# Performance work log

Measured on AMD Instinct MI355X. Metric: run time of the kernel, lower is better.

The kernel has to match this reference:

```python
import jax, jax.numpy as jnp
import numpy as np

B, T, D = 4, 2048, 2048
NUM_HEADS = 16
NUM_KV_HEADS = 4
HEAD_DIM = D // NUM_HEADS  # 128
KV_GROUPS = NUM_HEADS // NUM_KV_HEADS  # 4
ROPE_THETA = 10000.0


def _rope_tables(seq_len, head_dim, theta):
    inv_freq = 1.0 / theta ** (jnp.arange(0, head_dim, 2, dtype=jnp.float32) / head_dim)
    t = jnp.arange(seq_len, dtype=jnp.float32)
    freqs = jnp.outer(t, inv_freq)  # (T, head_dim//2)
    return jnp.cos(freqs), jnp.sin(freqs)


def _apply_rotary(x, cos, sin):
    # x: (B, H, T, d); cos/sin: (T, d//2)
    d = x.shape[-1]
    x1, x2 = x[..., : d // 2], x[..., d // 2:]
    c = cos[None, None, :, :]
    s = sin[None, None, :, :]
    return jnp.concatenate([x1 * c - x2 * s, x1 * s + x2 * c], axis=-1)


def setup_inputs() -> dict:
    key = jax.random.key(0)
    kx, kq, kk, kv, ko = jax.random.split(key, 5)
    scale = 1.0 / np.sqrt(D)
    return {
        "x": jax.random.normal(kx, (B, T, D), dtype=jnp.float32),
        "Wq": jax.random.normal(kq, (NUM_HEADS * HEAD_DIM, D), dtype=jnp.float32) * scale,
        "Wk": jax.random.normal(kk, (NUM_KV_HEADS * HEAD_DIM, D), dtype=jnp.float32) * scale,
        "Wv": jax.random.normal(kv, (NUM_KV_HEADS * HEAD_DIM, D), dtype=jnp.float32) * scale,
        "Wo": jax.random.normal(ko, (D, D), dtype=jnp.float32) * scale,
    }


def reference(x, Wq, Wk, Wv, Wo):
    Bc, Tc, Dc = x.shape
    # projections (Linear with weight (out,in): y = x @ W.T)
    q = (x @ Wq.T).reshape(Bc, Tc, NUM_HEADS, HEAD_DIM).transpose(0, 2, 1, 3)
    k = (x @ Wk.T).reshape(Bc, Tc, NUM_KV_HEADS, HEAD_DIM).transpose(0, 2, 1, 3)
    v = (x @ Wv.T).reshape(Bc, Tc, NUM_KV_HEADS, HEAD_DIM).transpose(0, 2, 1, 3)

    cos, sin = _rope_tables(Tc, HEAD_DIM, ROPE_THETA)
    q = _apply_rotary(q, cos, sin)
    k = _apply_rotary(k, cos, sin)

    # grouped-query attention: broadcast KV heads instead of repeat_interleave
    # q: (B, kvH, G, T, d); k,v: (B, kvH, T, d)
    qg = q.reshape(Bc, NUM_KV_HEADS, KV_GROUPS, Tc, HEAD_DIM)
    scores = jnp.einsum("bkgtd,bksd->bkgts", qg, k) / jnp.sqrt(jnp.float32(HEAD_DIM))
    causal = jnp.tril(jnp.ones((Tc, Tc), dtype=bool))
    scores = jnp.where(causal[None, None, None], scores, jnp.float32(-jnp.inf))
    attn = jax.nn.softmax(scores, axis=-1)
    out = jnp.einsum("bkgts,bksd->bkgtd", attn, v)  # (B, kvH, G, T, d)
    out = out.reshape(Bc, NUM_HEADS, Tc, HEAD_DIM).transpose(0, 2, 1, 3).reshape(Bc, Tc, Dc)
    return out @ Wo.T
```

## Files before the change

kernel.cpp:

```cpp
#include <hip/hip_runtime.h>
#include <stdint.h>

#define B_ 4
#define T_ 2048
#define D_ 2048
#define NH_ 16
#define NKV_ 4
#define HD_ 128
#define QKVN 3072
#define QSCALE_ 0.1275174334161689f

typedef unsigned short u16;
typedef __attribute__((ext_vector_type(8))) short short8;
typedef __attribute__((ext_vector_type(4))) float floatx4;

typedef __attribute__((address_space(1))) void* gas_p;
typedef __attribute__((address_space(3))) void* las_p;

__device__ __forceinline__ u16 f2bf(float f) {
  union { float f; uint32_t u; } a; a.f = f;
  uint32_t r = a.u + 0x7fffu + ((a.u >> 16) & 1u);
  return (u16)(r >> 16);
}
__device__ __forceinline__ float bf2f(u16 u) {
  union { uint32_t u; float f; } a; a.u = ((uint32_t)u) << 16;
  return a.f;
}
__device__ __forceinline__ void gl_lds16(const u16* g, u16* l) {
  __builtin_amdgcn_global_load_lds((gas_p)g, (las_p)l, 16, 0, 0);
}

__global__ void cvt_kernel(const float* __restrict__ in, u16* __restrict__ out, int n) {
  int i = blockIdx.x * 256 + threadIdx.x;
  if (i * 4 >= n) return;
  float4 v = ((const float4*)in)[i];
  union { u16 u[4]; uint2 v2; } o;
  o.u[0] = f2bf(v.x); o.u[1] = f2bf(v.y); o.u[2] = f2bf(v.z); o.u[3] = f2bf(v.w);
  ((uint2*)out)[i] = o.v2;
}

__global__ void rope_tables_kernel(float* __restrict__ tabs) {
  int i = blockIdx.x * 256 + threadIdx.x;
  if (i >= T_ * 64) return;
  int t = i >> 6, d = i & 63;
  float inv = powf(10000.0f, -(float)d / 64.0f);
  float f = (float)t * inv;
  tabs[i] = cosf(f);
  tabs[T_ * 64 + i] = sinf(f);
}

__global__ void rope_q_kernel(const u16* __restrict__ qkv, const float* __restrict__ tabs,
                              u16* __restrict__ q_r) {
  int i = blockIdx.x * 256 + threadIdx.x;
  if (i >= B_ * T_ * NH_ * 64) return;
  int d = i & 63;
  int h = (i >> 6) & 15;
  int t = (i >> 10) & 2047;
  int b = i >> 21;
  size_t row = (size_t)(b * T_ + t) * QKVN + h * HD_;
  float x1 = bf2f(qkv[row + d]);
  float x2 = bf2f(qkv[row + d + 64]);
  float c = tabs[t * 64 + d];
  float s = tabs[T_ * 64 + t * 64 + d];
  size_t ob = ((size_t)(b * NH_ + h) * T_ + t) * HD_;
  q_r[ob + d] = f2bf((x1 * c - x2 * s) * QSCALE_);
  q_r[ob + d + 64] = f2bf((x1 * s + x2 * c) * QSCALE_);
}

__global__ void rope_k_kernel(const u16* __restrict__ qkv, const float* __restrict__ tabs,
                              u16* __restrict__ k_r) {
  int i = blockIdx.x * 256 + threadIdx.x;
  if (i >= B_ * T_ * NKV_ * 64) return;
  int d = i & 63;
  int kh = (i >> 6) & 3;
  int t = (i >> 8) & 2047;
  int b = i >> 19;
  size_t row = (size_t)(b * T_ + t) * QKVN + D_ + kh * HD_;
  float x1 = bf2f(qkv[row + d]);
  float x2 = bf2f(qkv[row + d + 64]);
  float c = tabs[t * 64 + d];
  float s = tabs[T_ * 64 + t * 64 + d];
  size_t ob = ((size_t)(b * NKV_ + kh) * T_ + t) * HD_;
  k_r[ob + d] = f2bf(x1 * c - x2 * s);
  k_r[ob + d + 64] = f2bf(x1 * s + x2 * c);
}

__global__ void v_trans_kernel(const u16* __restrict__ qkv, u16* __restrict__ v_t) {
  __shared__ u16 tile[64 * 128];
  int bk = blockIdx.y;
  int b = bk >> 2, kh = bk & 3;
  int t0 = blockIdx.x * 64;
#pragma unroll
  for (int rep = 0; rep < 32; rep++) {
    int idx = rep * 256 + threadIdx.x;
    int tt = idx >> 7, d = idx & 127;
    tile[idx] = qkv[(size_t)(b * T_ + t0 + tt) * QKVN + D_ + 512 + kh * HD_ + d];
  }
  __syncthreads();
#pragma unroll
  for (int rep = 0; rep < 32; rep++) {
    int idx = rep * 256 + threadIdx.x;
    int d = idx >> 6, tt = idx & 63;
    v_t[((size_t)bk * HD_ + d) * T_ + t0 + tt] = tile[tt * 128 + d];
  }
}

template <int OUTF32>
__global__ __launch_bounds__(256)
void gemm_bt(const u16* __restrict__ A, const u16* __restrict__ Bm,
             void* __restrict__ Cv, int M, int N, int K) {
  __shared__ u16 As[128 * 64];
  __shared__ u16 Bs[128 * 64];
  const int tid = threadIdx.x;
  const int wave = tid >> 6, lane = tid & 63;
  const int l16 = lane & 15, quad = lane >> 4;
  const int m0 = blockIdx.y * 128, n0 = blockIdx.x * 128;
  const int wm = (wave >> 1) * 64, wn = (wave & 1) * 64;

  floatx4 acc[4][4];
#pragma unroll
  for (int i = 0; i < 4; i++)
#pragma unroll
    for (int j = 0; j < 4; j++)
#pragma unroll
      for (int r = 0; r < 4; r++) acc[i][j][r] = 0.0f;

  const u16* gA[4]; const u16* gB[4]; u16* lA[4]; u16* lB[4];
#pragma unroll
  for (int rep = 0; rep < 4; rep++) {
    int u = rep * 256 + tid;
    int row = u >> 3;
    int ks = (u & 7) ^ (row & 7);
    gA[rep] = A + (size_t)(m0 + row) * K + ks * 8;
    gB[rep] = Bm + (size_t)(n0 + row) * K + ks * 8;
    lA[rep] = &As[u * 8];
    lB[rep] = &Bs[u * 8];
  }

  for (int k0 = 0; k0 < K; k0 += 64) {
#pragma unroll
    for (int rep = 0; rep < 4; rep++) {
      gl_lds16(gA[rep] + k0, lA[rep]);
      gl_lds16(gB[rep] + k0, lB[rep]);
    }
    __syncthreads();
#pragma unroll
    for (int kc = 0; kc < 2; kc++) {
      const int kq = (kc * 4 + quad) ^ (l16 & 7);
      short8 af[4], bfv[4];
#pragma unroll
      for (int i = 0; i < 4; i++)
        af[i] = *(const short8*)(As + ((wm + i * 16 + l16) * 8 + kq) * 8);
#pragma unroll
      for (int j = 0; j < 4; j++)
        bfv[j] = *(const short8*)(Bs + ((wn + j * 16 + l16) * 8 + kq) * 8);
#pragma unroll
      for (int i = 0; i < 4; i++)
#pragma unroll
        for (int j = 0; j < 4; j++)
          acc[i][j] = __builtin_amdgcn_mfma_f32_16x16x32_bf16(af[i], bfv[j], acc[i][j], 0, 0, 0);
    }
    __syncthreads();
  }
#pragma unroll
  for (int i = 0; i < 4; i++)
#pragma unroll
    for (int j = 0; j < 4; j++)
#pragma unroll
      for (int r = 0; r < 4; r++) {
        int m = m0 + wm + i * 16 + quad * 4 + r;
        int n = n0 + wn + j * 16 + l16;
        if (OUTF32)
          ((float*)Cv)[(size_t)m * N + n] = acc[i][j][r];
        else
          ((u16*)Cv)[(size_t)m * N + n] = f2bf(acc[i][j][r]);
      }
}

__global__ __launch_bounds__(256)
void attn_fused(const u16* __restrict__ q_r, const u16* __restrict__ k_r,
                const u16* __restrict__ v_t, u16* __restrict__ outp) {
  __shared__ u16 Ks[64 * 128];
  __shared__ u16 Vs[64 * 128];
  __shared__ u16 Ps[4][32 * 64];
  const int tid = threadIdx.x;
  const int wave = tid >> 6, lane = tid & 63;
  const int l16 = lane & 15, quad = lane >> 4;
  const int bh = blockIdx.y;
  const int b = bh >> 4, h = bh & 15;
  const int kh = h >> 2;

  const u16* qhead = q_r + (size_t)bh * T_ * HD_;
  const u16* khead = k_r + (size_t)(b * NKV_ + kh) * T_ * HD_;
  const u16* vhead = v_t + (size_t)(b * NKV_ + kh) * HD_ * T_;

  int uu[4], kv_j[4], kv_kb[4], v_jo[4], v_k2[4], nn16[4], qq[4];
#pragma unroll
  for (int rep = 0; rep < 4; rep++) {
    int u = rep * 256 + tid;
    uu[rep] = u;
    nn16[rep] = u & 15; qq[rep] = (u >> 4) & 3;
    kv_j[rep] = (u >> 6) & 3; kv_kb[rep] = (u >> 8) & 3;
    v_jo[rep] = (u >> 6) & 7; v_k2[rep] = (u >> 9) & 1;
  }

  const short8 ones = { 0x3F80, 0x3F80, 0x3F80, 0x3F80, 0x3F80, 0x3F80, 0x3F80, 0x3F80 };
  char* psb = (char*)&Ps[wave][0];
  const int swz = (l16 & 7) << 4;

  for (int pass = 0; pass < 2; pass++) {
    const int qtile = pass ? (15 - (int)blockIdx.x) : (int)blockIdx.x;
    const int qbase = qtile * 128;
    const int ntiles = 2 * qtile + 2;

    short8 qf[2][4];
#pragma unroll
    for (int i = 0; i < 2; i++) {
      int t = qbase + wave * 32 + i * 16 + l16;
#pragma unroll
      for (int kb = 0; kb < 4; kb++)
        qf[i][kb] = *(const short8*)(qhead + (size_t)t * HD_ + kb * 32 + quad * 8);
    }

    const u16* kg[4]; const u16* vg[4]; u16* kl[4]; u16* vl[4];
#pragma unroll
    for (int rep = 0; rep < 4; rep++) {
      kg[rep] = khead + (size_t)(kv_j[rep] * 16 + nn16[rep]) * HD_ + kv_kb[rep] * 32 + qq[rep] * 8;
      vg[rep] = vhead + (size_t)(v_jo[rep] * 16 + nn16[rep]) * T_ + v_k2[rep] * 32 + qq[rep] * 8;
      kl[rep] = &Ks[uu[rep] * 8];
      vl[rep] = &Vs[uu[rep] * 8];
    }

    floatx4 acc_o[2][8];
    floatx4 acc_l[2];
#pragma unroll
    for (int i = 0; i < 2; i++) {
#pragma unroll
      for (int jo = 0; jo < 8; jo++)
#pragma unroll
        for (int r = 0; r < 4; r++) acc_o[i][jo][r] = 0.0f;
#pragma unroll
      for (int r = 0; r < 4; r++) acc_l[i][r] = 0.0f;
    }

    for (int tile = 0; tile < ntiles; tile++) {
      const int kv0 = tile * 64;
#pragma unroll
      for (int rep = 0; rep < 4; rep++) {
        gl_lds16(kg[rep], kl[rep]);
        gl_lds16(vg[rep], vl[rep]);
        kg[rep] += 64 * HD_;
        vg[rep] += 64;
      }
      __syncthreads();

      floatx4 s_acc[2][4];
#pragma unroll
      for (int i = 0; i < 2; i++)
#pragma unroll
        for (int j = 0; j < 4; j++)
#pragma unroll
          for (int r = 0; r < 4; r++) s_acc[i][j][r] = 0.0f;
      __builtin_amdgcn_s_setprio(1);
#pragma unroll
      for (int kb = 0; kb < 4; kb++) {
        short8 bk[4];
#pragma unroll
        for (int j = 0; j < 4; j++)
          bk[j] = *(const short8*)(Ks + (((kb * 4 + j) * 4 + quad) * 16 + l16) * 8);
#pragma unroll
        for (int i = 0; i < 2; i++)
#pragma unroll
          for (int j = 0; j < 4; j++)
            s_acc[i][j] = __builtin_amdgcn_mfma_f32_16x16x32_bf16(bk[j], qf[i][kb], s_acc[i][j], 0, 0, 0);
      }
      __builtin_amdgcn_s_setprio(0);

      if (tile + 2 >= ntiles) {
#pragma unroll
        for (int i = 0; i < 2; i++) {
          const int qg = qbase + wave * 32 + i * 16 + l16;
          const int prow = i * 16 + l16;
#pragma unroll
          for (int j = 0; j < 4; j++) {
            const int kg0 = kv0 + j * 16 + quad * 4;
            float p0 = (kg0 + 0 > qg) ? 0.0f : exp2f(s_acc[i][j][0]);
            float p1 = (kg0 + 1 > qg) ? 0.0f : exp2f(s_acc[i][j][1]);
            float p2 = (kg0 + 2 > qg) ? 0.0f : exp2f(s_acc[i][j][2]);
            float p3 = (kg0 + 3 > qg) ? 0.0f : exp2f(s_acc[i][j][3]);
            uint32_t lo, hi;
            asm("v_cvt_pk_bf16_f32 %0, %1, %2" : "=v"(lo) : "v"(p0), "v"(p1));
            asm("v_cvt_pk_bf16_f32 %0, %1, %2" : "=v"(hi) : "v"(p2), "v"(p3));
            uint2 pk; pk.x = lo; pk.y = hi;
            *(uint2*)(psb + ((prow * 128 + j * 32 + quad * 8) ^ swz)) = pk;
          }
        }
      } else {
#pragma unroll
        for (int i = 0; i < 2; i++) {
          const int prow = i * 16 + l16;
#pragma unroll
          for (int j = 0; j < 4; j++) {
            float p0 = exp2f(s_acc[i][j][0]);
            float p1 = exp2f(s_acc[i][j][1]);
            float p2 = exp2f(s_acc[i][j][2]);
            float p3 = exp2f(s_acc[i][j][3]);
            uint32_t lo, hi;
            asm("v_cvt_pk_bf16_f32 %0, %1, %2" : "=v"(lo) : "v"(p0), "v"(p1));
            asm("v_cvt_pk_bf16_f32 %0, %1, %2" : "=v"(hi) : "v"(p2), "v"(p3));
            uint2 pk; pk.x = lo; pk.y = hi;
            *(uint2*)(psb + ((prow * 128 + j * 32 + quad * 8) ^ swz)) = pk;
          }
        }
      }

      __builtin_amdgcn_s_setprio(1);
#pragma unroll
      for (int k2 = 0; k2 < 2; k2++) {
        short8 ap[2];
#pragma unroll
        for (int i = 0; i < 2; i++) {
          const int prow = i * 16 + l16;
          ap[i] = *(const short8*)(psb + ((prow * 128 + k2 * 64 + quad * 16) ^ swz));
        }
#pragma unroll
        for (int jo = 0; jo < 8; jo++) {
          short8 bv = *(const short8*)(Vs + (((k2 * 8 + jo) * 4 + quad) * 16 + l16) * 8);
          acc_o[0][jo] = __builtin_amdgcn_mfma_f32_16x16x32_bf16(ap[0], bv, acc_o[0][jo], 0, 0, 0);
          acc_o[1][jo] = __builtin_amdgcn_mfma_f32_16x16x32_bf16(ap[1], bv, acc_o[1][jo], 0, 0, 0);
        }
        acc_l[0] = __builtin_amdgcn_mfma_f32_16x16x32_bf16(ap[0], ones, acc_l[0], 0, 0, 0);
        acc_l[1] = __builtin_amdgcn_mfma_f32_16x16x32_bf16(ap[1], ones, acc_l[1], 0, 0, 0);
      }
      __builtin_amdgcn_s_setprio(0);
      __syncthreads();
    }

#pragma unroll
    for (int i = 0; i < 2; i++)
#pragma unroll
      for (int r = 0; r < 4; r++) {
        const float inv = 1.0f / acc_l[i][r];
        const int t = qbase + wave * 32 + i * 16 + quad * 4 + r;
        u16* orow = outp + ((size_t)(b * T_ + t)) * D_ + h * HD_;
#pragma unroll
        for (int jo = 0; jo < 8; jo++)
          orow[jo * 16 + l16] = f2bf(acc_o[i][jo][r] * inv);
      }
    __syncthreads();
  }
}

extern "C" void kernel_launch(void* const* d_in, const int* in_sizes, int n_in,
                              void* d_out, int out_size, void* d_ws, size_t ws_size,
                              hipStream_t stream) {
  const float* x  = (const float*)d_in[0];
  const float* Wq = (const float*)d_in[1];
  const float* Wk = (const float*)d_in[2];
  const float* Wv = (const float*)d_in[3];
  const float* Wo = (const float*)d_in[4];

  char* ws = (char*)d_ws;
  u16* xbf  = (u16*)(ws);
  u16* attn = xbf;
  u16* qkv  = (u16*)(ws + 33554432);
  u16* wcat = (u16*)(ws + 83886080);
  u16* wobf = (u16*)(ws + 96468992);
  u16* qr   = (u16*)(ws + 104857600);
  u16* kr   = (u16*)(ws + 138412032);
  u16* vt   = (u16*)(ws + 146800640);
  float* tabs = (float*)(ws + 155189248);

  cvt_kernel<<<16384, 256, 0, stream>>>(x, xbf, 16777216);
  cvt_kernel<<<4096, 256, 0, stream>>>(Wq, wcat, 4194304);
  cvt_kernel<<<1024, 256, 0, stream>>>(Wk, wcat + 4194304, 1048576);
  cvt_kernel<<<1024, 256, 0, stream>>>(Wv, wcat + 5242880, 1048576);
  cvt_kernel<<<4096, 256, 0, stream>>>(Wo, wobf, 4194304);
  rope_tables_kernel<<<512, 256, 0, stream>>>(tabs);

  gemm_bt<0><<<dim3(24, 64), 256, 0, stream>>>(xbf, wcat, (void*)qkv, 8192, 3072, 2048);

  rope_q_kernel<<<32768, 256, 0, stream>>>(qkv, tabs, qr);
  rope_k_kernel<<<8192, 256, 0, stream>>>(qkv, tabs, kr);
  v_trans_kernel<<<dim3(32, 16), 256, 0, stream>>>(qkv, vt);

  attn_fused<<<dim3(8, 64), 256, 0, stream>>>(qr, kr, vt, attn);

  gemm_bt<1><<<dim3(16, 64), 256, 0, stream>>>(attn, wobf, d_out, 8192, 2048, 2048);
}
```

Before: 500.8 us.

## Use 256x256 double-buffered GEMM tiles with XCD-aware block swizzle

Replaces the 128x128 single-buffered projection GEMM with a 256x256 tile run by 512 threads (8 waves, each computing 128x64). The kernel double-buffers LDS so the next K-slice loads while the current one is multiplied, and drops one barrier per iteration. It also remaps block IDs so neighbouring tiles land on the same XCD, and raises wave priority around the MFMA burst. The goal is more reuse per loaded byte, better L2 locality and hidden load latency. In exchange, LDS use reaches 128 KB per block and register pressure rises, which limits occupancy, and the QKV GEMM grid shrinks to 384 blocks.

Measured after the change: 460.8 us. 1.09x faster.

```diff
diff --git a/kernel.cpp b/kernel.cpp
--- a/kernel.cpp
+++ b/kernel.cpp
@@ -106,64 +106,88 @@
 }
 
 template <int OUTF32>
-__global__ __launch_bounds__(256)
-void gemm_bt(const u16* __restrict__ A, const u16* __restrict__ Bm,
-             void* __restrict__ Cv, int M, int N, int K) {
-  __shared__ u16 As[128 * 64];
-  __shared__ u16 Bs[128 * 64];
+__global__ __launch_bounds__(512, 2)
+void gemm_bt256(const u16* __restrict__ A, const u16* __restrict__ Bm,
+                void* __restrict__ Cv, int M, int N, int K) {
+  __shared__ u16 As[2][256 * 64];
+  __shared__ u16 Bs[2][256 * 64];
   const int tid = threadIdx.x;
   const int wave = tid >> 6, lane = tid & 63;
   const int l16 = lane & 15, quad = lane >> 4;
-  const int m0 = blockIdx.y * 128, n0 = blockIdx.x * 128;
-  const int wm = (wave >> 1) * 64, wn = (wave & 1) * 64;
-
-  floatx4 acc[4][4];
-#pragma unroll
-  for (int i = 0; i < 4; i++)
+
+  const int gx = gridDim.x;
+  const int nwg = gx * gridDim.y;
+  const int orig = blockIdx.y * gx + blockIdx.x;
+  const int cpx = nwg >> 3;
+  const int swid = (orig & 7) * cpx + (orig >> 3);
+  const int m0 = (swid / gx) * 256, n0 = (swid % gx) * 256;
+  const int wm = (wave >> 2) * 128, wn = (wave & 3) * 64;
+
+  floatx4 acc[8][4];
+#pragma unroll
+  for (int i = 0; i < 8; i++)
 #pragma unroll
     for (int j = 0; j < 4; j++)
 #pragma unroll
       for (int r = 0; r < 4; r++) acc[i][j][r] = 0.0f;
 
-  const u16* gA[4]; const u16* gB[4]; u16* lA[4]; u16* lB[4];
+  const u16* gA[4]; const u16* gB[4];
+  u16* lA0[4]; u16* lA1[4]; u16* lB0[4]; u16* lB1[4];
 #pragma unroll
   for (int rep = 0; rep < 4; rep++) {
-    int u = rep * 256 + tid;
+    int u = rep * 512 + tid;
     int row = u >> 3;
     int ks = (u & 7) ^ (row & 7);
     gA[rep] = A + (size_t)(m0 + row) * K + ks * 8;
     gB[rep] = Bm + (size_t)(n0 + row) * K + ks * 8;
-    lA[rep] = &As[u * 8];
-    lB[rep] = &Bs[u * 8];
-  }
-
-  for (int k0 = 0; k0 < K; k0 += 64) {
-#pragma unroll
-    for (int rep = 0; rep < 4; rep++) {
-      gl_lds16(gA[rep] + k0, lA[rep]);
-      gl_lds16(gB[rep] + k0, lB[rep]);
-    }
+    lA0[rep] = &As[0][u * 8]; lA1[rep] = &As[1][u * 8];
+    lB0[rep] = &Bs[0][u * 8]; lB1[rep] = &Bs[1][u * 8];
+  }
+
+#pragma unroll
+  for (int rep = 0; rep < 4; rep++) {
+    gl_lds16(gA[rep], lA0[rep]);
+    gl_lds16(gB[rep], lB0[rep]);
+  }
+
+  const int NT = K >> 6;
+#pragma unroll 1
+  for (int kt = 0; kt < NT; kt++) {
+    const int cur = kt & 1;
     __syncthreads();
+    if (kt + 1 < NT) {
+#pragma unroll
+      for (int rep = 0; rep < 4; rep++) {
+        gl_lds16(gA[rep] + 64, cur ? lA0[rep] : lA1[rep]);
+        gl_lds16(gB[rep] + 64, cur ? lB0[rep] : lB1[rep]);
+        gA[rep] += 64; gB[rep] += 64;
+      }
+      __builtin_amdgcn_sched_barrier(0);
+    }
+    const u16* ab = &As[cur][0];
+    const u16* bb = &Bs[cur][0];
 #pragma unroll
     for (int kc = 0; kc < 2; kc++) {
       const int kq = (kc * 4 + quad) ^ (l16 & 7);
-      short8 af[4], bfv[4];
-#pragma unroll
-      for (int i = 0; i < 4; i++)
-        af[i] = *(const short8*)(As + ((wm + i * 16 + l16) * 8 + kq) * 8);
+      short8 af[8], bfv[4];
+#pragma unroll
+      for (int i = 0; i < 8; i++)
+        af[i] = *(const short8*)(ab + ((wm + i * 16 + l16) * 8 + kq) * 8);
 #pragma unroll
       for (int j = 0; j < 4; j++)
-        bfv[j] = *(const short8*)(Bs + ((wn + j * 16 + l16) * 8 + kq) * 8);
-#pragma unroll
-      for (int i = 0; i < 4; i++)
+        bfv[j] = *(const short8*)(bb + ((wn + j * 16 + l16) * 8 + kq) * 8);
+      __builtin_amdgcn_s_setprio(1);
+#pragma unroll
+      for (int i = 0; i < 8; i++)
 #pragma unroll
         for (int j = 0; j < 4; j++)
           acc[i][j] = __builtin_amdgcn_mfma_f32_16x16x32_bf16(af[i], bfv[j], acc[i][j], 0, 0, 0);
-    }
-    __syncthreads();
-  }
-#pragma unroll
-  for (int i = 0; i < 4; i++)
+      __builtin_amdgcn_s_setprio(0);
+    }
+  }
+
+#pragma unroll
+  for (int i = 0; i < 8; i++)
 #pragma unroll
     for (int j = 0; j < 4; j++)
 #pragma unroll
@@ -378,7 +402,7 @@
   cvt_kernel<<<4096, 256, 0, stream>>>(Wo, wobf, 4194304);
   rope_tables_kernel<<<512, 256, 0, stream>>>(tabs);
 
-  gemm_bt<0><<<dim3(24, 64), 256, 0, stream>>>(xbf, wcat, (void*)qkv, 8192, 3072, 2048);
+  gemm_bt256<0><<<dim3(12, 32), 512, 0, stream>>>(xbf, wcat, (void*)qkv, 8192, 3072, 2048);
 
   rope_q_kernel<<<32768, 256, 0, stream>>>(qkv, tabs, qr);
   rope_k_kernel<<<8192, 256, 0, stream>>>(qkv, tabs, kr);
@@ -386,5 +410,5 @@
 
   attn_fused<<<dim3(8, 64), 256, 0, stream>>>(qr, kr, vt, attn);
 
-  gemm_bt<1><<<dim3(16, 64), 256, 0, stream>>>(attn, wobf, d_out, 8192, 2048, 2048);
-}
+  gemm_bt256<1><<<dim3(8, 32), 512, 0, stream>>>(attn, wobf, d_out, 8192, 2048, 2048);
+}
```
